# Optimization experiments

Hardware: AMD Instinct MI355X
Metric: run time of the kernel (lower is better)

Reference implementation:

```python
import jax, jax.numpy as jnp
import numpy as np
from jax import lax


@jax.custom_vjp
def binarize(w):
    # sign binarization of weights (XNOR-style), STE gradient in bwd
    return jnp.sign(w)

def _bin_fwd(w):
    return jnp.sign(w), w

def _bin_bwd(w, g):
    # straight-through estimator, clipped to |w| <= 1
    return (g * (jnp.abs(w) <= 1.0).astype(g.dtype),)

binarize.defvjp(_bin_fwd, _bin_bwd)


def hardtanh(x):
    return jnp.clip(x, -1.0, 1.0)


def bconv(x, w, b):
    # x: NCHW, w: OIHW, valid padding, stride 1, binarized weights
    y = lax.conv_general_dilated(
        x, binarize(w), window_strides=(1, 1), padding='VALID',
        dimension_numbers=('NCHW', 'OIHW', 'NCHW'))
    return y + b[None, :, None, None]


def maxpool2(x):
    return lax.reduce_window(x, -jnp.inf, lax.max,
                             window_dimensions=(1, 1, 2, 2),
                             window_strides=(1, 1, 2, 2),
                             padding='VALID')


def setup_inputs() -> dict:
    key = jax.random.key(0)
    ks = jax.random.split(key, 11)
    f32 = jnp.float32
    sc = 0.1  # keep weights inside the STE clip region mostly
    return {
        'x':  jax.random.normal(ks[0], (2048, 3, 32, 32), f32),
        'w1': jax.random.normal(ks[1], (100, 3, 5, 5), f32) * sc,
        'b1': jax.random.normal(ks[2], (100,), f32) * sc,
        'w2': jax.random.normal(ks[3], (16, 100, 5, 5), f32) * sc,
        'b2': jax.random.normal(ks[4], (16,), f32) * sc,
        'w3': jax.random.normal(ks[5], (120, 400), f32) * sc,
        'b3': jax.random.normal(ks[6], (120,), f32) * sc,
        'w4': jax.random.normal(ks[7], (84, 120), f32) * sc,
        'b4': jax.random.normal(ks[8], (84,), f32) * sc,
        'w5': jax.random.normal(ks[9], (10, 84), f32) * sc,
        'b5': jax.random.normal(ks[10], (10,), f32) * sc,
    }


def reference(x, w1, b1, w2, b2, w3, b3, w4, b4, w5, b5):
    h = maxpool2(hardtanh(bconv(x, w1, b1)))          # [B,100,14,14]
    h = maxpool2(hardtanh(bconv(h, w2, b2)))          # [B,16,5,5]
    h = h.reshape(h.shape[0], 16 * 5 * 5)             # [B,400]
    h = hardtanh(h @ binarize(w3).T + b3)             # [B,120]
    h = hardtanh(h @ binarize(w4).T + b4)             # [B,84]
    return h @ binarize(w5).T + b5                    # [B,10]
```

## Files before the change

### kernel.cpp

```cpp
#include <hip/hip_runtime.h>
#include <hip/hip_bf16.h>
#include <hip/hip_fp16.h>

typedef _Float16 f16x8 __attribute__((ext_vector_type(8)));
typedef float f32x4 __attribute__((ext_vector_type(4)));

union B8 { uint4 u; f16x8 h; };

__device__ __forceinline__ float htanh(float v) {
    return fminf(1.f, fmaxf(-1.f, v));
}
__device__ __forceinline__ unsigned short f2h(float f) {
    __half h = __float2half(f);
    return *reinterpret_cast<unsigned short*>(&h);
}
__device__ __forceinline__ float sxor(float h, float w) {
    return __uint_as_float(__float_as_uint(h) ^ (__float_as_uint(w) & 0x80000000u));
}

#define WSA1_OFF 102400
#define H2_OFF   138240

__global__ __launch_bounds__(256) void bn_pack(
    const float* __restrict__ w1, uint4* __restrict__ wsA1,
    const float* __restrict__ w2, uint4* __restrict__ wsA2)
{
    if (blockIdx.x < 9) {
        int t = blockIdx.x * 256 + threadIdx.x;
        if (t >= 2240) return;
        int lane = t & 63;
        int kk = (t >> 6) % 5;
        int m  = t / 320;
        int oc = m * 16 + (lane & 15), g = lane >> 4;
        unsigned int d[4];
        #pragma unroll
        for (int r = 0; r < 4; ++r) {
            int c, ky, kx; bool tv;
            if (kk < 4) { int rr = kk * 4 + g; tv = rr < 15; c = rr % 3; ky = rr / 3; kx = r; }
            else        { int s  = g * 4 + r;  tv = s  < 15; c = s  % 3; ky = s  / 3; kx = 4; }
            unsigned int v = 0u;
            if (tv && oc < 100) {
                float wv = w1[((oc * 3 + c) * 5 + ky) * 5 + kx];
                unsigned int sg = wv > 0.f ? 0x3C00u : (wv < 0.f ? 0xBC00u : 0u);
                v = sg | (sg << 16);
            }
            d[r] = v;
        }
        wsA1[t] = make_uint4(d[0], d[1], d[2], d[3]);
    } else {
        int t = (blockIdx.x - 9) * 256 + threadIdx.x;
        int lane = t & 63;
        int kk = (t >> 6) & 3;
        int s = t >> 8;
        int oc = lane & 15, g = lane >> 4;
        unsigned int d[4];
        #pragma unroll
        for (int r = 0; r < 4; ++r) {
            unsigned int u[2];
            #pragma unroll
            for (int h = 0; h < 2; ++h) {
                int ic = kk * 32 + g * 8 + r * 2 + h;
                unsigned int v = 0u;
                if (ic < 100) {
                    float wv = w2[(oc * 100 + ic) * 25 + s];
                    v = wv > 0.f ? 0x3C00u : (wv < 0.f ? 0xBC00u : 0u);
                }
                u[h] = v;
            }
            d[r] = u[0] | (u[1] << 16);
        }
        wsA2[t] = make_uint4(d[0], d[1], d[2], d[3]);
    }
}

template<int MC>
__device__ __forceinline__ void conv1_group(
    const unsigned int* __restrict__ sxu, const uint4* __restrict__ wsA1,
    const float* b1s, unsigned short* ht, int lane, int g, int col,
    int ntStart, int mBase)
{
    f16x8 a[MC][5];
    #pragma unroll
    for (int mi = 0; mi < MC; ++mi)
        #pragma unroll
        for (int kk = 0; kk < 5; ++kk) {
            B8 t; t.u = wsA1[((mBase + mi) * 5 + kk) * 64 + lane];
            a[mi][kk] = t.h;
        }

    const int g37 = g * 37, g148 = g * 148 + 4;

    for (int nt = ntStart; nt < 13; nt += 4) {
        const int w = nt * 16 + col;
        const bool valid = w < 196;
        const int wc = valid ? w : 195;
        const int wy = wc / 14, wx = wc - wy * 14;
        const unsigned int* bt = sxu + wy * 222 + wx * 2;
        const unsigned int* b0  = bt + g37;
        const unsigned int* blx = bt + g148;

        f32x4 mx[MC];
        #pragma unroll
        for (int pass = 0; pass < 4; ++pass) {
            const int q = (pass >> 1) * 111 + (pass & 1);

            f32x4 acc[MC];
            #pragma unroll
            for (int kk = 0; kk < 5; ++kk) {
                B8 bb;
                if (kk < 4) {
                    const unsigned int* bk = b0 + kk * 148;
                    bb.u = make_uint4(bk[q], bk[q + 1], bk[q + 2], bk[q + 3]);
                } else {
                    bb.u = make_uint4(blx[q], blx[q + 37], blx[q + 74], blx[q + 111]);
                }
                #pragma unroll
                for (int mi = 0; mi < MC; ++mi) {
                    f32x4 c0 = (kk == 0) ? (f32x4){0.f, 0.f, 0.f, 0.f} : acc[mi];
                    acc[mi] = __builtin_amdgcn_mfma_f32_16x16x32_f16(a[mi][kk], bb.h, c0, 0, 0, 0);
                }
            }
            #pragma unroll
            for (int mi = 0; mi < MC; ++mi) {
                if (pass == 0) {
                    mx[mi] = acc[mi];
                } else {
                    #pragma unroll
                    for (int r = 0; r < 4; ++r)
                        mx[mi][r] = fmaxf(mx[mi][r], acc[mi][r]);
                }
            }
        }

        if (valid) {
            #pragma unroll
            for (int mi = 0; mi < MC; ++mi) {
                const int oc0 = (mBase + mi) * 16 + g * 4;
                if (oc0 < 104) {
                    float4 bias = *(const float4*)&b1s[oc0];
                    unsigned short o0 = f2h(htanh(mx[mi][0] + bias.x));
                    unsigned short o1 = f2h(htanh(mx[mi][1] + bias.y));
                    unsigned short o2 = f2h(htanh(mx[mi][2] + bias.z));
                    unsigned short o3 = f2h(htanh(mx[mi][3] + bias.w));
                    uint2 d;
                    d.x = (unsigned int)o0 | ((unsigned int)o1 << 16);
                    d.y = (unsigned int)o2 | ((unsigned int)o3 << 16);
                    *(uint2*)(ht + w * 120 + oc0) = d;
                }
            }
        }
    }
}

__global__ __launch_bounds__(256, 2) void bn_convs(
    const float* __restrict__ x, const uint4* __restrict__ wsA1,
    const unsigned short* __restrict__ wsA2,
    const float* __restrict__ b1, const float* __restrict__ b2,
    float* __restrict__ h2)
{
    __shared__ __align__(16) unsigned int sxu[3584];
    __shared__ __align__(16) unsigned short ht[23616];
    __shared__ float b1s[112];
    const int img = blockIdx.x;
    const int tid = threadIdx.x;
    const int lane = tid & 63, wv = tid >> 6;

    {
        uint4* z = (uint4*)sxu;
        for (int i = tid; i < 896; i += 256) z[i] = make_uint4(0u, 0u, 0u, 0u);
        unsigned int* htw = (unsigned int*)ht;
        for (int i = tid; i < 1616; i += 256) {
            int wrd;
            if (i < 1568) { int row = i >> 3; wrd = row * 60 + 52 + (i & 7); }
            else          { wrd = 11760 + (i - 1568); }
            htw[wrd] = 0u;
        }
    }
    __syncthreads();

    {
        const float4* xg = (const float4*)(x + (size_t)img * 3072);
        for (int i = tid; i < 768; i += 256) {
            float4 v = xg[i];
            float vv[4] = {v.x, v.y, v.z, v.w};
            unsigned int u[4];
            #pragma unroll
            for (int q = 0; q < 4; ++q) {
                __half h = __float2half(vv[q]);
                float rs = vv[q] - __half2float(h);
                __half rl = __float2half(rs);
                u[q] = (unsigned int)*(unsigned short*)&h |
                       ((unsigned int)*(unsigned short*)&rl << 16);
            }
            int c = i >> 8, y = (i >> 3) & 31, q4 = i & 7;
            int base = 111 * y + 37 * c + 4 * q4;
            sxu[base]     = u[0];
            sxu[base + 1] = u[1];
            sxu[base + 2] = u[2];
            sxu[base + 3] = u[3];
        }
        if (tid < 112) b1s[tid] = (tid < 100) ? b1[tid] : 0.f;
    }
    __syncthreads();

    const int g = lane >> 4;
    const int col = lane & 15;

    const int s0 = (wv + (img & 3)) & 3;
    conv1_group<4>(sxu, wsA1, b1s, ht, lane, g, col, s0, 0);
    conv1_group<3>(sxu, wsA1, b1s, ht, lane, g, col, s0, 4);
    __syncthreads();

    int bc[7];
    #pragma unroll
    for (int t = 0; t < 7; ++t) {
        int P = t * 16 + col;
        int Pc = P < 100 ? P : 99;
        bc[t] = ((Pc / 10) * 14 + (Pc % 10)) * 120 + g * 8;
    }
    f32x4 acc[7];
    #pragma unroll
    for (int t = 0; t < 7; ++t) acc[t] = (f32x4){0.f, 0.f, 0.f, 0.f};

    const f16x8* wsAv = (const f16x8*)wsA2;
    const int ko = wv * 32;
    {
        f16x8 a2[13];
        #pragma unroll
        for (int j = 0; j < 13; ++j)
            a2[j] = wsAv[((j * 4 + wv) << 6) | lane];
        #pragma unroll
        for (int s = 0; s < 13; ++s) {
            const int off = ((s / 5) * 14 + (s % 5)) * 120 + ko;
            #pragma unroll
            for (int t = 0; t < 7; ++t) {
                f16x8 bb = *(const f16x8*)&ht[bc[t] + off];
                acc[t] = __builtin_amdgcn_mfma_f32_16x16x32_f16(a2[s], bb, acc[t], 0, 0, 0);
            }
        }
    }
    {
        f16x8 a2[12];
        #pragma unroll
        for (int j = 0; j < 12; ++j)
            a2[j] = wsAv[(((13 + j) * 4 + wv) << 6) | lane];
        #pragma unroll
        for (int s = 13; s < 25; ++s) {
            const int off = ((s / 5) * 14 + (s % 5)) * 120 + ko;
            #pragma unroll
            for (int t = 0; t < 7; ++t) {
                f16x8 bb = *(const f16x8*)&ht[bc[t] + off];
                acc[t] = __builtin_amdgcn_mfma_f32_16x16x32_f16(a2[s - 13], bb, acc[t], 0, 0, 0);
            }
        }
    }
    __syncthreads();

    float* pc = (float*)ht;
    #pragma unroll
    for (int t = 0; t < 7; ++t)
        #pragma unroll
        for (int r = 0; r < 4; ++r)
            pc[(((wv * 7 + t) * 16) + (g * 4 + r)) * 16 + col] = acc[t][r];
    __syncthreads();

    float* y = (float*)ht + 7168;
    for (int i = tid; i < 1792; i += 256) {
        int t = i >> 8, rem = i & 255;
        int oc = rem >> 4, c2 = rem & 15;
        int P = t * 16 + c2;
        if (P < 100) {
            int idx = (t * 16 + oc) * 16 + c2;
            float v = pc[idx] + pc[1792 + idx] + pc[3584 + idx] + pc[5376 + idx];
            y[oc * 100 + P] = htanh(v + b2[oc]);
        }
    }
    __syncthreads();

    for (int t2 = tid; t2 < 400; t2 += 256) {
        int oc = t2 / 25, pp = t2 - oc * 25;
        int ppy = pp / 5, ppx = pp - ppy * 5;
        int base = oc * 100 + ppy * 20 + ppx * 2;
        float m = fmaxf(fmaxf(y[base], y[base + 1]),
                        fmaxf(y[base + 10], y[base + 11]));
        h2[(size_t)img * 400 + t2] = m;
    }
}

__global__ __launch_bounds__(256) void bn_fc(
    const float* __restrict__ h2,
    const float* __restrict__ w3, const float* __restrict__ b3,
    const float* __restrict__ w4, const float* __restrict__ b4,
    const float* __restrict__ w5, const float* __restrict__ b5,
    float* __restrict__ out)
{
    __shared__ float sh2[4 * 404];
    __shared__ float sh3[4 * 124];
    __shared__ float sh4[4 * 88];
    const int b0 = blockIdx.x * 4;
    const int tid = threadIdx.x;

    for (int i = tid; i < 1600; i += 256) {
        int s = i / 400, k = i - s * 400;
        sh2[s * 404 + k] = h2[(size_t)(b0 + s) * 400 + k];
    }
    __syncthreads();

    for (int t = tid; t < 480; t += 256) {
        int o = t >> 2, s = t & 3;
        const float4* wr = (const float4*)(w3 + o * 400);
        const float4* hr = (const float4*)&sh2[s * 404];
        float a0 = 0.f, a1 = 0.f, a2 = 0.f, a3 = 0.f;
        #pragma unroll 5
        for (int k = 0; k < 100; ++k) {
            float4 w = wr[k], h = hr[k];
            a0 += sxor(h.x, w.x); a1 += sxor(h.y, w.y);
            a2 += sxor(h.z, w.z); a3 += sxor(h.w, w.w);
        }
        sh3[s * 124 + o] = htanh(b3[o] + ((a0 + a1) + (a2 + a3)));
    }
    __syncthreads();

    for (int t = tid; t < 336; t += 256) {
        int o = t >> 2, s = t & 3;
        const float4* wr = (const float4*)(w4 + o * 120);
        const float4* hr = (const float4*)&sh3[s * 124];
        float a0 = 0.f, a1 = 0.f, a2 = 0.f, a3 = 0.f;
        #pragma unroll
        for (int k = 0; k < 30; ++k) {
            float4 w = wr[k], h = hr[k];
            a0 += sxor(h.x, w.x); a1 += sxor(h.y, w.y);
            a2 += sxor(h.z, w.z); a3 += sxor(h.w, w.w);
        }
        sh4[s * 88 + o] = htanh(b4[o] + ((a0 + a1) + (a2 + a3)));
    }
    __syncthreads();

    for (int t = tid; t < 40; t += 256) {
        int o = t >> 2, s = t & 3;
        const float4* wr = (const float4*)(w5 + o * 84);
        const float4* hr = (const float4*)&sh4[s * 88];
        float a0 = 0.f, a1 = 0.f, a2 = 0.f, a3 = 0.f;
        #pragma unroll
        for (int k = 0; k < 21; ++k) {
            float4 w = wr[k], h = hr[k];
            a0 += sxor(h.x, w.x); a1 += sxor(h.y, w.y);
            a2 += sxor(h.z, w.z); a3 += sxor(h.w, w.w);
        }
        out[(size_t)(b0 + s) * 10 + o] = b5[o] + ((a0 + a1) + (a2 + a3));
    }
}

extern "C" void kernel_launch(void* const* d_in, const int* in_sizes, int n_in,
                              void* d_out, int out_size, void* d_ws, size_t ws_size,
                              hipStream_t stream) {
    const float* x  = (const float*)d_in[0];
    const float* w1 = (const float*)d_in[1];
    const float* b1 = (const float*)d_in[2];
    const float* w2 = (const float*)d_in[3];
    const float* b2 = (const float*)d_in[4];
    const float* w3 = (const float*)d_in[5];
    const float* b3 = (const float*)d_in[6];
    const float* w4 = (const float*)d_in[7];
    const float* b4 = (const float*)d_in[8];
    const float* w5 = (const float*)d_in[9];
    const float* b5 = (const float*)d_in[10];
    float* out = (float*)d_out;

    unsigned short* wsA2 = (unsigned short*)d_ws;
    uint4* wsA1          = (uint4*)((char*)d_ws + WSA1_OFF);
    float* h2            = (float*)((char*)d_ws + H2_OFF);

    hipLaunchKernelGGL(bn_pack, dim3(34), dim3(256), 0, stream,
                       w1, wsA1, w2, (uint4*)wsA2);
    hipLaunchKernelGGL(bn_convs, dim3(2048), dim3(256), 0, stream,
                       x, wsA1, wsA2, b1, b2, h2);
    hipLaunchKernelGGL(bn_fc, dim3(512), dim3(256), 0, stream, h2,
                       w3, b3, w4, b4, w5, b5, out);
}
```

Baseline: 115.8 us.

## Fuse fully-connected layers into conv kernel and widen pooled-map row stride

Moves the three binarized fully-connected layers into the per-image conv kernel, so the pooled 400-float features stay in shared memory instead of round-tripping through global memory, and one kernel launch goes away. The conv1 output tile is re-laid out with an 18-wide row stride and fully zeroed up front, replacing the scattered zeroing of padding. In exchange, each block now runs the FC layers for a single image with only up to 120 threads active, and rereads w3/w4/w5 per image rather than amortising across 4 images. The larger LDS footprint may also reduce occupancy.

```diff
diff --git a/kernel.cpp b/kernel.cpp
--- a/kernel.cpp
+++ b/kernel.cpp
@@ -19,7 +19,6 @@
 }
 
 #define WSA1_OFF 102400
-#define H2_OFF   138240
 
 __global__ __launch_bounds__(256) void bn_pack(
     const float* __restrict__ w1, uint4* __restrict__ wsA1,
@@ -73,6 +72,8 @@
     }
 }
 
+#define HT_HALVES 29952
+
 template<int MC>
 __device__ __forceinline__ void conv1_group(
     const unsigned int* __restrict__ sxu, const uint4* __restrict__ wsA1,
@@ -133,6 +134,7 @@
         }
 
         if (valid) {
+            const int sig = wy * 18 + wx;
             #pragma unroll
             for (int mi = 0; mi < MC; ++mi) {
                 const int oc0 = (mBase + mi) * 16 + g * 4;
@@ -145,7 +147,7 @@
                     uint2 d;
                     d.x = (unsigned int)o0 | ((unsigned int)o1 << 16);
                     d.y = (unsigned int)o2 | ((unsigned int)o3 << 16);
-                    *(uint2*)(ht + w * 120 + oc0) = d;
+                    *(uint2*)(ht + sig * 120 + oc0) = d;
                 }
             }
         }
@@ -156,10 +158,13 @@
     const float* __restrict__ x, const uint4* __restrict__ wsA1,
     const unsigned short* __restrict__ wsA2,
     const float* __restrict__ b1, const float* __restrict__ b2,
-    float* __restrict__ h2)
+    const float* __restrict__ w3, const float* __restrict__ b3,
+    const float* __restrict__ w4, const float* __restrict__ b4,
+    const float* __restrict__ w5, const float* __restrict__ b5,
+    float* __restrict__ out)
 {
     __shared__ __align__(16) unsigned int sxu[3584];
-    __shared__ __align__(16) unsigned short ht[23616];
+    __shared__ __align__(16) unsigned short ht[HT_HALVES];
     __shared__ float b1s[112];
     const int img = blockIdx.x;
     const int tid = threadIdx.x;
@@ -168,13 +173,8 @@
     {
         uint4* z = (uint4*)sxu;
         for (int i = tid; i < 896; i += 256) z[i] = make_uint4(0u, 0u, 0u, 0u);
-        unsigned int* htw = (unsigned int*)ht;
-        for (int i = tid; i < 1616; i += 256) {
-            int wrd;
-            if (i < 1568) { int row = i >> 3; wrd = row * 60 + 52 + (i & 7); }
-            else          { wrd = 11760 + (i - 1568); }
-            htw[wrd] = 0u;
-        }
+        uint4* zh = (uint4*)ht;
+        for (int i = tid; i < 3744; i += 256) zh[i] = make_uint4(0u, 0u, 0u, 0u);
     }
     __syncthreads();
 
@@ -216,7 +216,7 @@
     for (int t = 0; t < 7; ++t) {
         int P = t * 16 + col;
         int Pc = P < 100 ? P : 99;
-        bc[t] = ((Pc / 10) * 14 + (Pc % 10)) * 120 + g * 8;
+        bc[t] = ((Pc / 10) * 18 + (Pc % 10)) * 120 + g * 8;
     }
     f32x4 acc[7];
     #pragma unroll
@@ -231,7 +231,7 @@
             a2[j] = wsAv[((j * 4 + wv) << 6) | lane];
         #pragma unroll
         for (int s = 0; s < 13; ++s) {
-            const int off = ((s / 5) * 14 + (s % 5)) * 120 + ko;
+            const int off = ((s / 5) * 18 + (s % 5)) * 120 + ko;
             #pragma unroll
             for (int t = 0; t < 7; ++t) {
                 f16x8 bb = *(const f16x8*)&ht[bc[t] + off];
@@ -246,7 +246,7 @@
             a2[j] = wsAv[(((13 + j) * 4 + wv) << 6) | lane];
         #pragma unroll
         for (int s = 13; s < 25; ++s) {
-            const int off = ((s / 5) * 14 + (s % 5)) * 120 + ko;
+            const int off = ((s / 5) * 18 + (s % 5)) * 120 + ko;
             #pragma unroll
             for (int t = 0; t < 7; ++t) {
                 f16x8 bb = *(const f16x8*)&ht[bc[t] + off];
@@ -277,39 +277,22 @@
     }
     __syncthreads();
 
+    float* sh2 = (float*)ht + 8768;
     for (int t2 = tid; t2 < 400; t2 += 256) {
         int oc = t2 / 25, pp = t2 - oc * 25;
         int ppy = pp / 5, ppx = pp - ppy * 5;
         int base = oc * 100 + ppy * 20 + ppx * 2;
         float m = fmaxf(fmaxf(y[base], y[base + 1]),
                         fmaxf(y[base + 10], y[base + 11]));
-        h2[(size_t)img * 400 + t2] = m;
-    }
-}
-
-__global__ __launch_bounds__(256) void bn_fc(
-    const float* __restrict__ h2,
-    const float* __restrict__ w3, const float* __restrict__ b3,
-    const float* __restrict__ w4, const float* __restrict__ b4,
-    const float* __restrict__ w5, const float* __restrict__ b5,
-    float* __restrict__ out)
-{
-    __shared__ float sh2[4 * 404];
-    __shared__ float sh3[4 * 124];
-    __shared__ float sh4[4 * 88];
-    const int b0 = blockIdx.x * 4;
-    const int tid = threadIdx.x;
-
-    for (int i = tid; i < 1600; i += 256) {
-        int s = i / 400, k = i - s * 400;
-        sh2[s * 404 + k] = h2[(size_t)(b0 + s) * 400 + k];
-    }
-    __syncthreads();
-
-    for (int t = tid; t < 480; t += 256) {
-        int o = t >> 2, s = t & 3;
-        const float4* wr = (const float4*)(w3 + o * 400);
-        const float4* hr = (const float4*)&sh2[s * 404];
+        sh2[t2] = m;
+    }
+    __syncthreads();
+
+    float* sh3 = (float*)ht + 9168;
+    float* sh4 = (float*)ht + 9288;
+    if (tid < 120) {
+        const float4* wr = (const float4*)(w3 + tid * 400);
+        const float4* hr = (const float4*)sh2;
         float a0 = 0.f, a1 = 0.f, a2 = 0.f, a3 = 0.f;
         #pragma unroll 5
         for (int k = 0; k < 100; ++k) {
@@ -317,14 +300,12 @@
             a0 += sxor(h.x, w.x); a1 += sxor(h.y, w.y);
             a2 += sxor(h.z, w.z); a3 += sxor(h.w, w.w);
         }
-        sh3[s * 124 + o] = htanh(b3[o] + ((a0 + a1) + (a2 + a3)));
-    }
-    __syncthreads();
-
-    for (int t = tid; t < 336; t += 256) {
-        int o = t >> 2, s = t & 3;
-        const float4* wr = (const float4*)(w4 + o * 120);
-        const float4* hr = (const float4*)&sh3[s * 124];
+        sh3[tid] = htanh(b3[tid] + ((a0 + a1) + (a2 + a3)));
+    }
+    __syncthreads();
+    if (tid < 84) {
+        const float4* wr = (const float4*)(w4 + tid * 120);
+        const float4* hr = (const float4*)sh3;
         float a0 = 0.f, a1 = 0.f, a2 = 0.f, a3 = 0.f;
         #pragma unroll
         for (int k = 0; k < 30; ++k) {
@@ -332,14 +313,12 @@
             a0 += sxor(h.x, w.x); a1 += sxor(h.y, w.y);
             a2 += sxor(h.z, w.z); a3 += sxor(h.w, w.w);
         }
-        sh4[s * 88 + o] = htanh(b4[o] + ((a0 + a1) + (a2 + a3)));
-    }
-    __syncthreads();
-
-    for (int t = tid; t < 40; t += 256) {
-        int o = t >> 2, s = t & 3;
-        const float4* wr = (const float4*)(w5 + o * 84);
-        const float4* hr = (const float4*)&sh4[s * 88];
+        sh4[tid] = htanh(b4[tid] + ((a0 + a1) + (a2 + a3)));
+    }
+    __syncthreads();
+    if (tid < 10) {
+        const float4* wr = (const float4*)(w5 + tid * 84);
+        const float4* hr = (const float4*)sh4;
         float a0 = 0.f, a1 = 0.f, a2 = 0.f, a3 = 0.f;
         #pragma unroll
         for (int k = 0; k < 21; ++k) {
@@ -347,7 +326,7 @@
             a0 += sxor(h.x, w.x); a1 += sxor(h.y, w.y);
             a2 += sxor(h.z, w.z); a3 += sxor(h.w, w.w);
         }
-        out[(size_t)(b0 + s) * 10 + o] = b5[o] + ((a0 + a1) + (a2 + a3));
+        out[(size_t)img * 10 + tid] = b5[tid] + ((a0 + a1) + (a2 + a3));
     }
 }
 
@@ -369,12 +348,9 @@
 
     unsigned short* wsA2 = (unsigned short*)d_ws;
     uint4* wsA1          = (uint4*)((char*)d_ws + WSA1_OFF);
-    float* h2            = (float*)((char*)d_ws + H2_OFF);
 
     hipLaunchKernelGGL(bn_pack, dim3(34), dim3(256), 0, stream,
                        w1, wsA1, w2, (uint4*)wsA2);
     hipLaunchKernelGGL(bn_convs, dim3(2048), dim3(256), 0, stream,
-                       x, wsA1, wsA2, b1, b2, h2);
-    hipLaunchKernelGGL(bn_fc, dim3(512), dim3(256), 0, stream, h2,
-                       w3, b3, w4, b4, w5, b5, out);
-}
+                       x, wsA1, wsA2, b1, b2, w3, b3, w4, b4, w5, b5, out);
+}
```

Measured after the change: 121.2 us. 4.7% more time.

## Double conv block to 512 threads and split conv work across eight waves

Applied to the files above, without the earlier changes.

The fused conv kernel now runs 8 waves per image instead of 4. Conv1 output-channel groups go to separate wave halves, and conv2 position tiles are split between two wave groups (tile 3 is computed by both). The intermediate pooled buffer uses an 18-wide row pitch, so it is zeroed fully with vector stores instead of selective padding writes. This aims to raise wave-level parallelism and latency hiding per CU, at the cost of more LDS per block and some duplicated MFMA work.

```diff
diff --git a/kernel.cpp b/kernel.cpp
--- a/kernel.cpp
+++ b/kernel.cpp
@@ -73,6 +73,8 @@
     }
 }
 
+#define HT_HALVES 29952
+
 template<int MC>
 __device__ __forceinline__ void conv1_group(
     const unsigned int* __restrict__ sxu, const uint4* __restrict__ wsA1,
@@ -133,6 +135,7 @@
         }
 
         if (valid) {
+            const int sig = wy * 18 + wx;
             #pragma unroll
             for (int mi = 0; mi < MC; ++mi) {
                 const int oc0 = (mBase + mi) * 16 + g * 4;
@@ -145,21 +148,21 @@
                     uint2 d;
                     d.x = (unsigned int)o0 | ((unsigned int)o1 << 16);
                     d.y = (unsigned int)o2 | ((unsigned int)o3 << 16);
-                    *(uint2*)(ht + w * 120 + oc0) = d;
-                }
-            }
-        }
-    }
-}
-
-__global__ __launch_bounds__(256, 2) void bn_convs(
+                    *(uint2*)(ht + sig * 120 + oc0) = d;
+                }
+            }
+        }
+    }
+}
+
+__global__ __launch_bounds__(512) void bn_convs(
     const float* __restrict__ x, const uint4* __restrict__ wsA1,
     const unsigned short* __restrict__ wsA2,
     const float* __restrict__ b1, const float* __restrict__ b2,
     float* __restrict__ h2)
 {
     __shared__ __align__(16) unsigned int sxu[3584];
-    __shared__ __align__(16) unsigned short ht[23616];
+    __shared__ __align__(16) unsigned short ht[HT_HALVES];
     __shared__ float b1s[112];
     const int img = blockIdx.x;
     const int tid = threadIdx.x;
@@ -167,20 +170,15 @@
 
     {
         uint4* z = (uint4*)sxu;
-        for (int i = tid; i < 896; i += 256) z[i] = make_uint4(0u, 0u, 0u, 0u);
-        unsigned int* htw = (unsigned int*)ht;
-        for (int i = tid; i < 1616; i += 256) {
-            int wrd;
-            if (i < 1568) { int row = i >> 3; wrd = row * 60 + 52 + (i & 7); }
-            else          { wrd = 11760 + (i - 1568); }
-            htw[wrd] = 0u;
-        }
+        for (int i = tid; i < 896; i += 512) z[i] = make_uint4(0u, 0u, 0u, 0u);
+        uint4* zh = (uint4*)ht;
+        for (int i = tid; i < 3744; i += 512) zh[i] = make_uint4(0u, 0u, 0u, 0u);
     }
     __syncthreads();
 
     {
         const float4* xg = (const float4*)(x + (size_t)img * 3072);
-        for (int i = tid; i < 768; i += 256) {
+        for (int i = tid; i < 768; i += 512) {
             float4 v = xg[i];
             float vv[4] = {v.x, v.y, v.z, v.w};
             unsigned int u[4];
@@ -206,36 +204,38 @@
     const int g = lane >> 4;
     const int col = lane & 15;
 
-    const int s0 = (wv + (img & 3)) & 3;
-    conv1_group<4>(sxu, wsA1, b1s, ht, lane, g, col, s0, 0);
-    conv1_group<3>(sxu, wsA1, b1s, ht, lane, g, col, s0, 4);
-    __syncthreads();
-
-    int bc[7];
+    const int s0 = ((wv & 3) + (img & 3)) & 3;
+    if (wv < 4) conv1_group<4>(sxu, wsA1, b1s, ht, lane, g, col, s0, 0);
+    else        conv1_group<3>(sxu, wsA1, b1s, ht, lane, g, col, s0, 4);
+    __syncthreads();
+
+    const int kk2 = wv & 3;
+    const int tBase = (wv >> 2) ? 3 : 0;
+    int bc[4];
     #pragma unroll
-    for (int t = 0; t < 7; ++t) {
-        int P = t * 16 + col;
+    for (int ti = 0; ti < 4; ++ti) {
+        int P = (tBase + ti) * 16 + col;
         int Pc = P < 100 ? P : 99;
-        bc[t] = ((Pc / 10) * 14 + (Pc % 10)) * 120 + g * 8;
-    }
-    f32x4 acc[7];
+        bc[ti] = ((Pc / 10) * 18 + (Pc % 10)) * 120 + g * 8;
+    }
+    f32x4 acc[4];
     #pragma unroll
-    for (int t = 0; t < 7; ++t) acc[t] = (f32x4){0.f, 0.f, 0.f, 0.f};
+    for (int ti = 0; ti < 4; ++ti) acc[ti] = (f32x4){0.f, 0.f, 0.f, 0.f};
 
     const f16x8* wsAv = (const f16x8*)wsA2;
-    const int ko = wv * 32;
+    const int ko = kk2 * 32;
     {
         f16x8 a2[13];
         #pragma unroll
         for (int j = 0; j < 13; ++j)
-            a2[j] = wsAv[((j * 4 + wv) << 6) | lane];
+            a2[j] = wsAv[((j * 4 + kk2) << 6) | lane];
         #pragma unroll
         for (int s = 0; s < 13; ++s) {
-            const int off = ((s / 5) * 14 + (s % 5)) * 120 + ko;
-            #pragma unroll
-            for (int t = 0; t < 7; ++t) {
-                f16x8 bb = *(const f16x8*)&ht[bc[t] + off];
-                acc[t] = __builtin_amdgcn_mfma_f32_16x16x32_f16(a2[s], bb, acc[t], 0, 0, 0);
+            const int off = ((s / 5) * 18 + (s % 5)) * 120 + ko;
+            #pragma unroll
+            for (int ti = 0; ti < 4; ++ti) {
+                f16x8 bb = *(const f16x8*)&ht[bc[ti] + off];
+                acc[ti] = __builtin_amdgcn_mfma_f32_16x16x32_f16(a2[s], bb, acc[ti], 0, 0, 0);
             }
         }
     }
@@ -243,14 +243,14 @@
         f16x8 a2[12];
         #pragma unroll
         for (int j = 0; j < 12; ++j)
-            a2[j] = wsAv[(((13 + j) * 4 + wv) << 6) | lane];
+            a2[j] = wsAv[(((13 + j) * 4 + kk2) << 6) | lane];
         #pragma unroll
         for (int s = 13; s < 25; ++s) {
-            const int off = ((s / 5) * 14 + (s % 5)) * 120 + ko;
-            #pragma unroll
-            for (int t = 0; t < 7; ++t) {
-                f16x8 bb = *(const f16x8*)&ht[bc[t] + off];
-                acc[t] = __builtin_amdgcn_mfma_f32_16x16x32_f16(a2[s - 13], bb, acc[t], 0, 0, 0);
+            const int off = ((s / 5) * 18 + (s % 5)) * 120 + ko;
+            #pragma unroll
+            for (int ti = 0; ti < 4; ++ti) {
+                f16x8 bb = *(const f16x8*)&ht[bc[ti] + off];
+                acc[ti] = __builtin_amdgcn_mfma_f32_16x16x32_f16(a2[s - 13], bb, acc[ti], 0, 0, 0);
             }
         }
     }
@@ -258,14 +258,16 @@
 
     float* pc = (float*)ht;
     #pragma unroll
-    for (int t = 0; t < 7; ++t)
+    for (int ti = 0; ti < 4; ++ti) {
+        int t = tBase + ti;
         #pragma unroll
         for (int r = 0; r < 4; ++r)
-            pc[(((wv * 7 + t) * 16) + (g * 4 + r)) * 16 + col] = acc[t][r];
+            pc[((kk2 * 7 + t) * 16 + (g * 4 + r)) * 16 + col] = acc[ti][r];
+    }
     __syncthreads();
 
     float* y = (float*)ht + 7168;
-    for (int i = tid; i < 1792; i += 256) {
+    for (int i = tid; i < 1792; i += 512) {
         int t = i >> 8, rem = i & 255;
         int oc = rem >> 4, c2 = rem & 15;
         int P = t * 16 + c2;
@@ -277,7 +279,7 @@
     }
     __syncthreads();
 
-    for (int t2 = tid; t2 < 400; t2 += 256) {
+    for (int t2 = tid; t2 < 400; t2 += 512) {
         int oc = t2 / 25, pp = t2 - oc * 25;
         int ppy = pp / 5, ppx = pp - ppy * 5;
         int base = oc * 100 + ppy * 20 + ppx * 2;
@@ -373,7 +375,7 @@
 
     hipLaunchKernelGGL(bn_pack, dim3(34), dim3(256), 0, stream,
                        w1, wsA1, w2, (uint4*)wsA2);
-    hipLaunchKernelGGL(bn_convs, dim3(2048), dim3(256), 0, stream,
+    hipLaunchKernelGGL(bn_convs, dim3(2048), dim3(512), 0, stream,
                        x, wsA1, wsA2, b1, b2, h2);
     hipLaunchKernelGGL(bn_fc, dim3(512), dim3(256), 0, stream, h2,
                        w3, b3, w4, b4, w5, b5, out);
```

After: 131.2 us. 1.13x slower.
